# Performance work log

Hardware: AMD Instinct MI355X
Metric: run time of the kernel (lower is better)

## Reference

```python
import jax, jax.numpy as jnp
import numpy as np

SIGMA = 0.5
EPS = 1e-7


def _offdiag(M):
    # M: [n, n] -> [n, n-1], row i keeps columns j != i (same order as
    # torch masked_select with (1 - eye) mask followed by view(n, n-1)).
    n = M.shape[0]
    j = jnp.arange(n - 1)
    cols = j[None, :] + (j[None, :] >= jnp.arange(n)[:, None]).astype(j.dtype)  # [n, n-1]
    return jnp.take_along_axis(M, cols, axis=1)


def _pairwise_neg_dist(features):
    # -||f_i - f_j||_2 with a grad-safe sqrt (diagonal is exactly 0; torch's
    # norm backward yields 0 there, so we guard the sqrt).
    diff = features[:, None, :] - features[None, :, :]          # [n, n, d]
    sq = jnp.sum(diff * diff, axis=-1)                          # [n, n]
    safe = jnp.where(sq > 0, sq, 1.0)
    return -jnp.where(sq > 0, jnp.sqrt(safe), 0.0)


def setup_inputs() -> dict:
    key = jax.random.key(0)
    k1, k2 = jax.random.split(key)
    feature = jax.random.normal(k1, (512, 512), dtype=jnp.float32)
    label = jax.random.uniform(k2, (512, 1), dtype=jnp.float32)
    return {"feature": feature, "label": label}


def reference(feature, label):
    n = feature.shape[0]
    # R[i, j] = sum_c |label_i - label_j|
    R = jnp.sum(jnp.abs(label[:, None, :] - label[None, :, :]), axis=-1)  # [n, n]

    F = _pairwise_neg_dist(feature) * SIGMA                               # [n, n]
    F_max = jax.lax.stop_gradient(jnp.max(F, axis=1, keepdims=True))
    F = F - F_max
    scaled_F = jax.nn.softmax(F, axis=1)                                  # [n, n]

    F_off = _offdiag(F)            # [n, n-1]
    S_off = _offdiag(scaled_F)     # [n, n-1]
    R_off = _offdiag(R)            # [n, n-1]

    # neg_mask[k, i, j] = (R_off[i, j] >= R_off[i, k]); here laid out [i, k, j].
    mask = (R_off[:, None, :] >= R_off[:, :, None]).astype(F.dtype)       # [n, n-1, n-1]
    denom = jnp.einsum('ikj,ij->ik', mask, S_off)                         # [n, n-1]

    pos_log_probs = F_off - jnp.log(denom + EPS)                          # [n, n-1]
    loss = -jnp.sum(pos_log_probs) / (n * (n - 1))
    return loss
```

## Files before the change

kernel.cpp:

```cpp
#include <hip/hip_runtime.h>
#include <math.h>

#define N 512
#define SIGMA 0.5f
#define EPS 1e-7f

typedef __attribute__((ext_vector_type(8))) short bf16x8;
typedef __attribute__((ext_vector_type(4))) float f32x4;

__device__ __forceinline__ unsigned short f2bf(float x) {
    unsigned int b = __float_as_uint(x);
    b += 0x7FFFu + ((b >> 16) & 1u);
    return (unsigned short)(b >> 16);
}

__global__ __launch_bounds__(512)
void setup_kernel(const float* __restrict__ feat,
                  const float* __restrict__ label,
                  unsigned short* __restrict__ featb,
                  float* __restrict__ sqn,
                  float* __restrict__ sl, int* __restrict__ sidx,
                  int* __restrict__ ipos, float* __restrict__ out) {
    const int t = threadIdx.x;
    if (blockIdx.x < 64) {
        const int wave = t >> 6, lane = t & 63;
        const int row = blockIdx.x * 8 + wave;
        const float* f = feat + (size_t)row * N;
        unsigned short* fb = featb + (size_t)row * N;
        float s = 0.f;
        #pragma unroll
        for (int sweep = 0; sweep < 2; ++sweep) {
            int c = sweep * 256 + lane * 4;
            float4 v = *(const float4*)(f + c);
            unsigned short b0 = f2bf(v.x), b1 = f2bf(v.y),
                           b2 = f2bf(v.z), b3 = f2bf(v.w);
            *(ushort4*)(fb + c) = make_ushort4(b0, b1, b2, b3);
            float r0 = __uint_as_float((unsigned int)b0 << 16);
            float r1 = __uint_as_float((unsigned int)b1 << 16);
            float r2 = __uint_as_float((unsigned int)b2 << 16);
            float r3 = __uint_as_float((unsigned int)b3 << 16);
            s += r0 * r0 + r1 * r1 + r2 * r2 + r3 * r3;
        }
        #pragma unroll
        for (int off = 32; off > 0; off >>= 1) s += __shfl_down(s, off);
        if (lane == 0) sqn[row] = s;
    } else {
        __shared__ __align__(16) float lab[N];
        const float lt = label[t];
        lab[t] = lt;
        if (t == 0) out[0] = 0.f;
        __syncthreads();
        int rank = 0;
        const float4* L4 = (const float4*)lab;
        #pragma unroll 8
        for (int j4 = 0; j4 < N / 4; ++j4) {
            float4 v = L4[j4];
            int j = j4 * 4;
            rank += ((v.x < lt) || (v.x == lt && (j + 0) < t)) ? 1 : 0;
            rank += ((v.y < lt) || (v.y == lt && (j + 1) < t)) ? 1 : 0;
            rank += ((v.z < lt) || (v.z == lt && (j + 2) < t)) ? 1 : 0;
            rank += ((v.w < lt) || (v.w == lt && (j + 3) < t)) ? 1 : 0;
        }
        sl[rank] = lt;
        sidx[rank] = t;
        ipos[t] = rank;
    }
}

__global__ void fmat_mfma_kernel(const unsigned short* __restrict__ featb,
                                 const float* __restrict__ sqn,
                                 float* __restrict__ Fm) {
    const int r0 = blockIdx.y * 16;
    const int c0 = blockIdx.x * 16;
    const int lane = threadIdx.x;
    const int m = lane & 15;
    const int kb = (lane >> 4) * 8;

    const unsigned short* arow = featb + (size_t)(r0 + m) * N + kb;
    const unsigned short* brow = featb + (size_t)(c0 + m) * N + kb;

    f32x4 acc = {0.f, 0.f, 0.f, 0.f};
    #pragma unroll
    for (int k0 = 0; k0 < N; k0 += 32) {
        bf16x8 a = *(const bf16x8*)(arow + k0);
        bf16x8 b = *(const bf16x8*)(brow + k0);
        acc = __builtin_amdgcn_mfma_f32_16x16x32_bf16(a, b, acc, 0, 0, 0);
    }

    const int col = c0 + (lane & 15);
    const int rowb = r0 + (lane >> 4) * 4;
    const float nc = sqn[col];
    #pragma unroll
    for (int r = 0; r < 4; ++r) {
        const int row = rowb + r;
        float sq = sqn[row] + nc - 2.f * acc[r];
        float v = (row == col) ? 0.f : -SIGMA * sqrtf(fmaxf(sq, 0.f));
        Fm[(size_t)row * N + col] = v;
    }
}

__global__ __launch_bounds__(512)
void row_kernel(const float* __restrict__ Fm,
                const float* __restrict__ label,
                const float* __restrict__ sl,
                const int* __restrict__ sidx,
                const int* __restrict__ ipos,
                float* __restrict__ out) {
    const int i = blockIdx.x;
    const int t = threadIdx.x;
    const int wave = t >> 6, lane = t & 63;

    __shared__ __align__(16) float ds_[N];
    __shared__ __align__(16) float Ss[N];
    __shared__ __align__(16) float Ps[N];
    __shared__ float red[8];
    __shared__ float wsum[8];

    const float li = label[i];
    const float f = Fm[(size_t)i * N + t];
    const float e = __expf(f);

    ds_[t] = fabsf(li - sl[t]);

    float z = e;
    #pragma unroll
    for (int off = 32; off > 0; off >>= 1) z += __shfl_xor(z, off);
    if (lane == 0) red[wave] = z;
    __syncthreads();
    const float Z = red[0] + red[1] + red[2] + red[3] +
                    red[4] + red[5] + red[6] + red[7];
    float S = e / Z;
    if (t == i) S = 0.f;
    Ss[t] = S;
    __syncthreads();

    float v = Ss[sidx[t]];
    #pragma unroll
    for (int off = 1; off < 64; off <<= 1) {
        float u = __shfl_up(v, off);
        if (lane >= off) v += u;
    }
    if (lane == 63) wsum[wave] = v;
    __syncthreads();
    float base = 0.f;
    #pragma unroll
    for (int w = 0; w < 8; ++w) base += (w < wave) ? wsum[w] : 0.f;
    Ps[t] = base + v;
    __syncthreads();

    const float total = Ps[N - 1];
    const int posi = ipos[i];
    const int pt = ipos[t];
    const float Rk = ds_[pt];

    int lo = 0, hi = posi + 1;
    while (lo < hi) { int mid = (lo + hi) >> 1; if (ds_[mid] < Rk) hi = mid; else lo = mid + 1; }
    const int La = lo;
    lo = posi; hi = N;
    while (lo < hi) { int mid = (lo + hi) >> 1; if (ds_[mid] >= Rk) hi = mid; else lo = mid + 1; }
    const int Rb = lo - 1;

    const float inner = ((Rb >= 0) ? Ps[Rb] : 0.f) - ((La > 0) ? Ps[La - 1] : 0.f);
    const float denom = total - inner;
    float part = (t == i) ? 0.f : (f - __logf(denom + EPS));

    #pragma unroll
    for (int off = 32; off > 0; off >>= 1) part += __shfl_xor(part, off);
    if (lane == 0) red[wave] = part;
    __syncthreads();
    if (t == 0) {
        float tot = red[0] + red[1] + red[2] + red[3] +
                    red[4] + red[5] + red[6] + red[7];
        atomicAdd(out, tot * (-1.f / ((float)N * (float)(N - 1))));
    }
}

extern "C" void kernel_launch(void* const* d_in, const int* in_sizes, int n_in,
                              void* d_out, int out_size, void* d_ws, size_t ws_size,
                              hipStream_t stream) {
    const float* feature = (const float*)d_in[0];
    const float* label   = (const float*)d_in[1];
    float* out = (float*)d_out;

    float* Fm             = (float*)d_ws;
    unsigned short* featb = (unsigned short*)(Fm + (size_t)N * N);
    float* sqn            = (float*)(featb + (size_t)N * N);
    float* sl             = sqn + N;
    int*   sidx           = (int*)(sl + N);
    int*   ipos           = sidx + N;

    setup_kernel<<<65, 512, 0, stream>>>(feature, label, featb, sqn,
                                         sl, sidx, ipos, out);
    {
        dim3 grid(N / 16, N / 16);
        fmat_mfma_kernel<<<grid, 64, 0, stream>>>(featb, sqn, Fm);
    }
    row_kernel<<<N, N, 0, stream>>>(Fm, label, sl, sidx, ipos, out);
}
```

Baseline: 87.37 us.

## Exploit distance-matrix symmetry and split setup into many small blocks

The distance matrix kernel now computes only lower-triangular 16x16 tiles (528 blocks instead of 1024) and writes each tile plus its transpose, using the symmetry of pairwise distances. The setup kernel is split into 520 single-wave blocks (one per feature row plus 8 label-ranking blocks) to spread the work across more CUs. The row kernel computes the label distance directly instead of through an indirect shared-memory lookup, and gains an occupancy hint. The transposed writes are float4 column stores that are less coalesced, and diagonal tiles are written twice.

```diff
diff --git a/kernel.cpp b/kernel.cpp
--- a/kernel.cpp
+++ b/kernel.cpp
@@ -13,18 +13,22 @@
     b += 0x7FFFu + ((b >> 16) & 1u);
     return (unsigned short)(b >> 16);
 }
-
-__global__ __launch_bounds__(512)
-void setup_kernel(const float* __restrict__ feat,
-                  const float* __restrict__ label,
-                  unsigned short* __restrict__ featb,
-                  float* __restrict__ sqn,
-                  float* __restrict__ sl, int* __restrict__ sidx,
-                  int* __restrict__ ipos, float* __restrict__ out) {
-    const int t = threadIdx.x;
-    if (blockIdx.x < 64) {
-        const int wave = t >> 6, lane = t & 63;
-        const int row = blockIdx.x * 8 + wave;
+__device__ __forceinline__ float bf2f(unsigned short h) {
+    return __uint_as_float((unsigned int)h << 16);
+}
+
+__global__ void convert_kernel(const float* __restrict__ feat,
+                               const float* __restrict__ label,
+                               unsigned short* __restrict__ featb,
+                               float* __restrict__ sqn,
+                               float* __restrict__ sl,
+                               int* __restrict__ sidx,
+                               int* __restrict__ ipos,
+                               float* __restrict__ out) {
+    const int lane = threadIdx.x;
+    if (blockIdx.x < 512) {
+        const int row = blockIdx.x;
+        if (row == 0 && lane == 0) out[0] = 0.f;
         const float* f = feat + (size_t)row * N;
         unsigned short* fb = featb + (size_t)row * N;
         float s = 0.f;
@@ -35,10 +39,7 @@
             unsigned short b0 = f2bf(v.x), b1 = f2bf(v.y),
                            b2 = f2bf(v.z), b3 = f2bf(v.w);
             *(ushort4*)(fb + c) = make_ushort4(b0, b1, b2, b3);
-            float r0 = __uint_as_float((unsigned int)b0 << 16);
-            float r1 = __uint_as_float((unsigned int)b1 << 16);
-            float r2 = __uint_as_float((unsigned int)b2 << 16);
-            float r3 = __uint_as_float((unsigned int)b3 << 16);
+            float r0 = bf2f(b0), r1 = bf2f(b1), r2 = bf2f(b2), r3 = bf2f(b3);
             s += r0 * r0 + r1 * r1 + r2 * r2 + r3 * r3;
         }
         #pragma unroll
@@ -46,10 +47,12 @@
         if (lane == 0) sqn[row] = s;
     } else {
         __shared__ __align__(16) float lab[N];
-        const float lt = label[t];
-        lab[t] = lt;
-        if (t == 0) out[0] = 0.f;
+        #pragma unroll
+        for (int q = 0; q < 2; ++q)
+            ((float4*)lab)[lane * 2 + q] = ((const float4*)label)[lane * 2 + q];
         __syncthreads();
+        const int t = (blockIdx.x - 512) * 64 + lane;
+        const float lt = lab[t];
         int rank = 0;
         const float4* L4 = (const float4*)lab;
         #pragma unroll 8
@@ -67,11 +70,18 @@
     }
 }
 
-__global__ void fmat_mfma_kernel(const unsigned short* __restrict__ featb,
-                                 const float* __restrict__ sqn,
-                                 float* __restrict__ Fm) {
-    const int r0 = blockIdx.y * 16;
-    const int c0 = blockIdx.x * 16;
+__global__ __launch_bounds__(64)
+void fmat_sym_kernel(const unsigned short* __restrict__ featb,
+                     const float* __restrict__ sqn,
+                     float* __restrict__ Fm) {
+    const int id = blockIdx.x;
+    int bi = (int)((sqrtf(8.f * (float)id + 1.f) - 1.f) * 0.5f);
+    while ((bi + 1) * (bi + 2) / 2 <= id) ++bi;
+    while (bi * (bi + 1) / 2 > id) --bi;
+    const int bj = id - bi * (bi + 1) / 2;
+
+    const int r0 = bi * 16;
+    const int c0 = bj * 16;
     const int lane = threadIdx.x;
     const int m = lane & 15;
     const int kb = (lane >> 4) * 8;
@@ -87,19 +97,23 @@
         acc = __builtin_amdgcn_mfma_f32_16x16x32_bf16(a, b, acc, 0, 0, 0);
     }
 
-    const int col = c0 + (lane & 15);
+    const int col = c0 + m;
     const int rowb = r0 + (lane >> 4) * 4;
     const float nc = sqn[col];
+    float v0_, v1_, v2_, v3_;
     #pragma unroll
     for (int r = 0; r < 4; ++r) {
         const int row = rowb + r;
         float sq = sqn[row] + nc - 2.f * acc[r];
         float v = (row == col) ? 0.f : -SIGMA * sqrtf(fmaxf(sq, 0.f));
         Fm[(size_t)row * N + col] = v;
-    }
-}
-
-__global__ __launch_bounds__(512)
+        if (r == 0) v0_ = v; else if (r == 1) v1_ = v;
+        else if (r == 2) v2_ = v; else v3_ = v;
+    }
+    *(float4*)(Fm + (size_t)col * N + rowb) = make_float4(v0_, v1_, v2_, v3_);
+}
+
+__global__ __launch_bounds__(512, 4)
 void row_kernel(const float* __restrict__ Fm,
                 const float* __restrict__ label,
                 const float* __restrict__ sl,
@@ -150,8 +164,7 @@
 
     const float total = Ps[N - 1];
     const int posi = ipos[i];
-    const int pt = ipos[t];
-    const float Rk = ds_[pt];
+    const float Rk = fabsf(li - label[t]);
 
     int lo = 0, hi = posi + 1;
     while (lo < hi) { int mid = (lo + hi) >> 1; if (ds_[mid] < Rk) hi = mid; else lo = mid + 1; }
@@ -189,11 +202,8 @@
     int*   sidx           = (int*)(sl + N);
     int*   ipos           = sidx + N;
 
-    setup_kernel<<<65, 512, 0, stream>>>(feature, label, featb, sqn,
-                                         sl, sidx, ipos, out);
-    {
-        dim3 grid(N / 16, N / 16);
-        fmat_mfma_kernel<<<grid, 64, 0, stream>>>(featb, sqn, Fm);
-    }
+    convert_kernel<<<520, 64, 0, stream>>>(feature, label, featb, sqn,
+                                           sl, sidx, ipos, out);
+    fmat_sym_kernel<<<528, 64, 0, stream>>>(featb, sqn, Fm);
     row_kernel<<<N, N, 0, stream>>>(Fm, label, sl, sidx, ipos, out);
 }
```

Result: faster. 84.65 us (-3.1%).
